# Kernel optimization log

Hardware: AMD Instinct MI355X
Metric: run time of the kernel (lower is better)

## Reference

```python
import jax, jax.numpy as jnp
import numpy as np

B, S, D, H, R, N, RK = 2, 2048, 1024, 16, 64, 32, 128
DH = D // H
EPS = 1e-5


def setup_inputs() -> dict:
    key = jax.random.key(0)
    ks = jax.random.split(key, 24)
    f = lambda i, shape, sc=1.0: jax.random.normal(ks[i], shape, dtype=jnp.float32) * sc
    sm = lambda i, shape: jax.nn.softmax(f(i, shape), axis=-1)
    return {
        'x': f(0, (B, S, D)),
        'f_qk': f(1, (N, D, R), 0.02), 'f_v': f(2, (N, D, R), 0.02),
        'r_qk': f(3, (N, R, D), 0.02), 'r_v': f(4, (N, R, D), 0.02),
        'f_know': f(5, (N, D, RK), 0.02), 'r_know': f(6, (N, RK, D), 0.02),
        'W_O': f(7, (D, D), 0.02),
        'gamma1': jnp.ones(D, jnp.float32), 'beta1': jnp.zeros(D, jnp.float32),
        'gamma2': jnp.ones(D, jnp.float32), 'beta2': jnp.zeros(D, jnp.float32),
        'w_fq': sm(8, (B, S, N)), 'w_fk': sm(9, (B, S, N)), 'w_fv': sm(10, (B, S, N)),
        'w_rq': sm(11, (B, S, N)), 'w_rk': sm(12, (B, S, N)), 'w_rv': sm(13, (B, S, N)),
        'w_know_f': sm(14, (B, S, N)), 'w_know_r': sm(15, (B, S, N)),
    }


def _ln(x, g, b):
    mu = jnp.mean(x, axis=-1, keepdims=True)
    var = jnp.mean(jnp.square(x - mu), axis=-1, keepdims=True)
    return g * (x - mu) * jax.lax.rsqrt(var + EPS) + b


def _feature(x, neurons, w):
    # x [B,S,D], neurons [N,D,R], w [B,S,N] -> [B,S,R]
    all_h = jnp.einsum('bsd,ndr->bsnr', x, neurons)
    return jnp.einsum('bsnr,bsn->bsr', all_h, w)


def _restore(h, neurons, w):
    # h [B,S,R], neurons [N,R,D], w [B,S,N] -> [B,S,D]
    # fuse: avoid materializing [B,S,N,D]; outer-product [B,S,N,R] is small
    t = w[..., None] * h[:, :, None, :]
    return jnp.einsum('bsnr,nrd->bsd', t, neurons)


def _causal_attn(Q, K, V):
    # Q,K,V: [B,H,S,DH]
    scale = 1.0 / jnp.sqrt(jnp.asarray(DH, Q.dtype))
    scores = jnp.einsum('bhqd,bhkd->bhqk', Q, K) * scale
    mask = jnp.tril(jnp.ones((S, S), bool))
    scores = jnp.where(mask, scores, jnp.asarray(-jnp.inf, scores.dtype))
    probs = jax.nn.softmax(scores, axis=-1)
    return jnp.einsum('bhqk,bhkd->bhqd', probs, V)


def reference(x, f_qk, f_v, r_qk, r_v, f_know, r_know, W_O,
              gamma1, beta1, gamma2, beta2,
              w_fq, w_fk, w_fv, w_rq, w_rk, w_rv, w_know_f, w_know_r):
    # --- attention circuit ---
    nx = _ln(x, gamma1, beta1)
    h_q = _feature(nx, f_qk, w_fq)
    h_k = _feature(nx, f_qk, w_fk)
    h_v = _feature(nx, f_v, w_fv)
    Q = _restore(h_q, r_qk, w_rq)
    K = _restore(h_k, r_qk, w_rk)
    V = _restore(h_v, r_v, w_rv)
    to_heads = lambda t: t.reshape(B, S, H, DH).transpose(0, 2, 1, 3)
    attn = _causal_attn(to_heads(Q), to_heads(K), to_heads(V))
    attn = attn.transpose(0, 2, 1, 3).reshape(B, S, D)
    attn_out = attn @ W_O.T  # nn.Linear(d_model, d_model, bias=False)
    x = x + attn_out
    # --- knowledge circuit ---
    nx2 = _ln(x, gamma2, beta2)
    h = _feature(nx2, f_know, w_know_f)
    know_out = _restore(h, r_know, w_know_r)
    x = x + know_out
    return x
```

## Files before the change

kernel.cpp:

```cpp
#include <hip/hip_runtime.h>
#include <stdint.h>


typedef __bf16 bf16x8 __attribute__((ext_vector_type(8)));
typedef float f32x4 __attribute__((ext_vector_type(4)));

__device__ __forceinline__ unsigned short f2b(float f) {
  union { float f; unsigned u; } v; v.f = f;
  unsigned u = v.u;
  unsigned r = (u + 0x7FFFu + ((u >> 16) & 1u)) >> 16;
  return (unsigned short)r;
}
__device__ __forceinline__ float b2f(unsigned short h) {
  union { unsigned u; float f; } v; v.u = ((unsigned)h) << 16;
  return v.f;
}
__device__ __forceinline__ unsigned pk2(float lo, float hi) {
  return (unsigned)f2b(lo) | ((unsigned)f2b(hi) << 16);
}

__global__ __launch_bounds__(256) void gemm_bt(
    const unsigned short* __restrict__ A, const unsigned short* __restrict__ Bt,
    const float* __restrict__ res, void* __restrict__ out,
    int M, int N, int K, int mode, int band) {
  __shared__ unsigned short lsA[128 * 64];
  __shared__ unsigned short lsB[128 * 64];
  const int tid = threadIdx.x;
  const int w = tid >> 6, lane = tid & 63;
  const int quad = lane >> 4, l16 = lane & 15;
  const int wr = w >> 1, wc = w & 1;
  int bx = blockIdx.x, by = blockIdx.y;
  if (band > 0) {
    const int bid = by * gridDim.x + bx;
    const int xcd = bid & 7, j = bid >> 3;
    by = xcd * band + j / gridDim.x;
    bx = j % gridDim.x;
  }
  const int row0 = by * 128;
  const int col0 = bx * 128;

  const int srow = w * 32 + (lane >> 3);
  const int scg = ((lane & 7) ^ (lane >> 3)) * 8;
  const unsigned short* ap = A + (size_t)(row0 + srow) * K + scg;
  const unsigned short* bp = Bt + (size_t)(col0 + srow) * K + scg;

  const f32x4 fz = {0.f, 0.f, 0.f, 0.f};
  f32x4 acc[4][4];
#pragma unroll
  for (int i = 0; i < 4; ++i)
#pragma unroll
    for (int j = 0; j < 4; ++j) acc[i][j] = fz;

  for (int k0 = 0; k0 < K; k0 += 64) {
#pragma unroll
    for (int i = 0; i < 4; ++i) {
      __builtin_amdgcn_global_load_lds(
          (const __attribute__((address_space(1))) unsigned int*)(ap + (size_t)i * 8 * K + k0),
          (__attribute__((address_space(3))) unsigned int*)&lsA[(w * 32 + i * 8) * 64],
          16, 0, 0);
      __builtin_amdgcn_global_load_lds(
          (const __attribute__((address_space(1))) unsigned int*)(bp + (size_t)i * 8 * K + k0),
          (__attribute__((address_space(3))) unsigned int*)&lsB[(w * 32 + i * 8) * 64],
          16, 0, 0);
    }
    __syncthreads();
#pragma unroll
    for (int kk = 0; kk < 2; ++kk) {
      bf16x8 af[4], bfr[4];
      const int sl = (((kk * 4 + quad) ^ (l16 & 7)) * 8);
#pragma unroll
      for (int mt = 0; mt < 4; ++mt)
        af[mt] = *(const bf16x8*)&lsA[(wr * 64 + mt * 16 + l16) * 64 + sl];
#pragma unroll
      for (int nt = 0; nt < 4; ++nt)
        bfr[nt] = *(const bf16x8*)&lsB[(wc * 64 + nt * 16 + l16) * 64 + sl];
#pragma unroll
      for (int mt = 0; mt < 4; ++mt)
#pragma unroll
        for (int nt = 0; nt < 4; ++nt)
          acc[mt][nt] = __builtin_amdgcn_mfma_f32_16x16x32_bf16(af[mt], bfr[nt], acc[mt][nt], 0, 0, 0);
    }
    __syncthreads();
  }

  const int rb = row0 + wr * 64;
  const int cb = col0 + wc * 64;
#pragma unroll
  for (int mt = 0; mt < 4; ++mt) {
#pragma unroll
    for (int nt = 0; nt < 4; ++nt) {
      const int r = rb + mt * 16 + quad * 4;
      const int c = cb + nt * 16 + l16;
#pragma unroll
      for (int i = 0; i < 4; ++i) {
        const float v = acc[mt][nt][i];
        const size_t idx = (size_t)(r + i) * N + c;
        if (mode == 0) ((float*)out)[idx] = v;
        else if (mode == 1) ((unsigned short*)out)[idx] = f2b(v);
        else if (mode == 2) ((float*)out)[idx] = v + res[idx];
        else ((unsigned short*)out)[(size_t)c * M + (r + i)] = f2b(v);
      }
    }
  }
}

__global__ __launch_bounds__(256) void gemm_ks2(
    const unsigned short* __restrict__ A, const unsigned short* __restrict__ Bt,
    float* __restrict__ p0, float* __restrict__ p1, int M, int N, int K) {
  __shared__ unsigned short lsA[128 * 64];
  __shared__ unsigned short lsB[128 * 64];
  const int tid = threadIdx.x;
  const int w = tid >> 6, lane = tid & 63;
  const int quad = lane >> 4, l16 = lane & 15;
  const int wr = w >> 1, wc = w & 1;
  const int nrow8 = (M / 128) >> 3;
  const int bid = blockIdx.y * gridDim.x + blockIdx.x;
  const int xcd = bid & 7, j = bid >> 3;
  const int by = xcd * nrow8 + j / (2 * gridDim.x);
  const int rem = j % (2 * gridDim.x);
  const int ks = rem / gridDim.x;
  const int bx = rem % gridDim.x;
  const int row0 = by * 128;
  const int col0 = bx * 128;
  const int kbeg = ks * (K >> 1), kend = kbeg + (K >> 1);

  const int srow = w * 32 + (lane >> 3);
  const int scg = ((lane & 7) ^ (lane >> 3)) * 8;
  const unsigned short* ap = A + (size_t)(row0 + srow) * K + scg;
  const unsigned short* bp = Bt + (size_t)(col0 + srow) * K + scg;

  const f32x4 fz = {0.f, 0.f, 0.f, 0.f};
  f32x4 acc[4][4];
#pragma unroll
  for (int i = 0; i < 4; ++i)
#pragma unroll
    for (int jj = 0; jj < 4; ++jj) acc[i][jj] = fz;

  for (int k0 = kbeg; k0 < kend; k0 += 64) {
#pragma unroll
    for (int i = 0; i < 4; ++i) {
      __builtin_amdgcn_global_load_lds(
          (const __attribute__((address_space(1))) unsigned int*)(ap + (size_t)i * 8 * K + k0),
          (__attribute__((address_space(3))) unsigned int*)&lsA[(w * 32 + i * 8) * 64],
          16, 0, 0);
      __builtin_amdgcn_global_load_lds(
          (const __attribute__((address_space(1))) unsigned int*)(bp + (size_t)i * 8 * K + k0),
          (__attribute__((address_space(3))) unsigned int*)&lsB[(w * 32 + i * 8) * 64],
          16, 0, 0);
    }
    __syncthreads();
#pragma unroll
    for (int kk = 0; kk < 2; ++kk) {
      bf16x8 af[4], bfr[4];
      const int sl = (((kk * 4 + quad) ^ (l16 & 7)) * 8);
#pragma unroll
      for (int mt = 0; mt < 4; ++mt)
        af[mt] = *(const bf16x8*)&lsA[(wr * 64 + mt * 16 + l16) * 64 + sl];
#pragma unroll
      for (int nt = 0; nt < 4; ++nt)
        bfr[nt] = *(const bf16x8*)&lsB[(wc * 64 + nt * 16 + l16) * 64 + sl];
#pragma unroll
      for (int mt = 0; mt < 4; ++mt)
#pragma unroll
        for (int nt = 0; nt < 4; ++nt)
          acc[mt][nt] = __builtin_amdgcn_mfma_f32_16x16x32_bf16(af[mt], bfr[nt], acc[mt][nt], 0, 0, 0);
    }
    __syncthreads();
  }

  float* out = ks ? p1 : p0;
  const int rb = row0 + wr * 64;
  const int cb = col0 + wc * 64;
#pragma unroll
  for (int mt = 0; mt < 4; ++mt) {
#pragma unroll
    for (int nt = 0; nt < 4; ++nt) {
      const int r = rb + mt * 16 + quad * 4;
      const int c = cb + nt * 16 + l16;
#pragma unroll
      for (int i = 0; i < 4; ++i)
        out[(size_t)(r + i) * N + c] = acc[mt][nt][i];
    }
  }
}

__global__ __launch_bounds__(256) void reduce_add3(
    const float* __restrict__ p0, const float* __restrict__ p1,
    const float* __restrict__ res, float* __restrict__ out, int n) {
  const int i = (blockIdx.x * 256 + threadIdx.x) * 4;
  if (i < n) {
    const f32x4 a = *(const f32x4*)&p0[i];
    const f32x4 b = *(const f32x4*)&p1[i];
    const f32x4 c = *(const f32x4*)&res[i];
    f32x4 o;
#pragma unroll
    for (int k = 0; k < 4; ++k) o[k] = a[k] + b[k] + c[k];
    *(f32x4*)&out[i] = o;
  }
}

__global__ __launch_bounds__(256) void gemm_qkv(
    const unsigned short* __restrict__ t_qk, const unsigned short* __restrict__ t_v,
    const unsigned short* __restrict__ r_qkT, const unsigned short* __restrict__ r_vT,
    unsigned short* __restrict__ QKbuf, unsigned short* __restrict__ VT) {
  __shared__ unsigned short lsA[128 * 64];
  __shared__ unsigned short lsB[128 * 64];
  const int K = 2048;
  const int bid = blockIdx.y * 8 + blockIdx.x;
  const int xcd = bid & 7, j = bid >> 3;
  const int r128 = xcd * 12 + (j >> 3);
  const bool isV = r128 >= 64;
  const unsigned short* A  = isV ? t_v : t_qk;
  const unsigned short* Bt = isV ? r_vT : r_qkT;
  const int row0 = (isV ? r128 - 64 : r128) * 128;
  const int col0 = (j & 7) * 128;
  const int tid = threadIdx.x;
  const int w = tid >> 6, lane = tid & 63;
  const int quad = lane >> 4, l16 = lane & 15;
  const int wr = w >> 1, wc = w & 1;

  const int srow = w * 32 + (lane >> 3);
  const int scg = ((lane & 7) ^ (lane >> 3)) * 8;
  const unsigned short* ap = A + (size_t)(row0 + srow) * K + scg;
  const unsigned short* bp = Bt + (size_t)(col0 + srow) * K + scg;

  const f32x4 fz = {0.f, 0.f, 0.f, 0.f};
  f32x4 acc[4][4];
#pragma unroll
  for (int i = 0; i < 4; ++i)
#pragma unroll
    for (int jj = 0; jj < 4; ++jj) acc[i][jj] = fz;

  for (int k0 = 0; k0 < K; k0 += 64) {
#pragma unroll
    for (int i = 0; i < 4; ++i) {
      __builtin_amdgcn_global_load_lds(
          (const __attribute__((address_space(1))) unsigned int*)(ap + (size_t)i * 8 * K + k0),
          (__attribute__((address_space(3))) unsigned int*)&lsA[(w * 32 + i * 8) * 64],
          16, 0, 0);
      __builtin_amdgcn_global_load_lds(
          (const __attribute__((address_space(1))) unsigned int*)(bp + (size_t)i * 8 * K + k0),
          (__attribute__((address_space(3))) unsigned int*)&lsB[(w * 32 + i * 8) * 64],
          16, 0, 0);
    }
    __syncthreads();
#pragma unroll
    for (int kk = 0; kk < 2; ++kk) {
      bf16x8 af[4], bfr[4];
      const int sl = (((kk * 4 + quad) ^ (l16 & 7)) * 8);
#pragma unroll
      for (int mt = 0; mt < 4; ++mt)
        af[mt] = *(const bf16x8*)&lsA[(wr * 64 + mt * 16 + l16) * 64 + sl];
#pragma unroll
      for (int nt = 0; nt < 4; ++nt)
        bfr[nt] = *(const bf16x8*)&lsB[(wc * 64 + nt * 16 + l16) * 64 + sl];
#pragma unroll
      for (int mt = 0; mt < 4; ++mt)
#pragma unroll
        for (int nt = 0; nt < 4; ++nt)
          acc[mt][nt] = __builtin_amdgcn_mfma_f32_16x16x32_bf16(af[mt], bfr[nt], acc[mt][nt], 0, 0, 0);
    }
    __syncthreads();
  }

  const int rb = row0 + wr * 64;
  const int cb = col0 + wc * 64;
#pragma unroll
  for (int mt = 0; mt < 4; ++mt) {
#pragma unroll
    for (int nt = 0; nt < 4; ++nt) {
      const int r = rb + mt * 16 + quad * 4;
      const int c = cb + nt * 16 + l16;
#pragma unroll
      for (int i = 0; i < 4; ++i) {
        const float v = acc[mt][nt][i];
        if (!isV) QKbuf[(size_t)(r + i) * 1024 + c] = f2b(v);
        else VT[(size_t)c * 4096 + (r + i)] = f2b(v);
      }
    }
  }
}

__global__ __launch_bounds__(256) void ln_kernel(
    const float* __restrict__ x, const float* __restrict__ g,
    const float* __restrict__ be, unsigned short* __restrict__ out) {
  __shared__ float sbuf[4];
  const int t = blockIdx.x, tid = threadIdx.x;
  const float* row = x + (size_t)t * 1024;
  float v[4], s = 0.f;
#pragma unroll
  for (int j = 0; j < 4; ++j) { v[j] = row[tid + j * 256]; s += v[j]; }
#pragma unroll
  for (int off = 32; off; off >>= 1) s += __shfl_xor(s, off);
  if ((tid & 63) == 0) sbuf[tid >> 6] = s;
  __syncthreads();
  const float mu = (sbuf[0] + sbuf[1] + sbuf[2] + sbuf[3]) * (1.f / 1024.f);
  __syncthreads();
  float ss = 0.f;
#pragma unroll
  for (int j = 0; j < 4; ++j) { const float d = v[j] - mu; ss += d * d; }
#pragma unroll
  for (int off = 32; off; off >>= 1) ss += __shfl_xor(ss, off);
  if ((tid & 63) == 0) sbuf[tid >> 6] = ss;
  __syncthreads();
  const float var = (sbuf[0] + sbuf[1] + sbuf[2] + sbuf[3]) * (1.f / 1024.f);
  const float rstd = rsqrtf(var + 1e-5f);
  unsigned short* orow = out + (size_t)t * 1024;
#pragma unroll
  for (int j = 0; j < 4; ++j) {
    const int c = tid + j * 256;
    orow[c] = f2b((v[j] - mu) * rstd * g[c] + be[c]);
  }
}

__global__ __launch_bounds__(256) void mix_attn(
    const unsigned short* __restrict__ all_h,
    const float* __restrict__ w_fq, const float* __restrict__ w_fk,
    const float* __restrict__ w_fv, const float* __restrict__ w_rq,
    const float* __restrict__ w_rk, const float* __restrict__ w_rv,
    unsigned short* __restrict__ t_qk, unsigned short* __restrict__ t_v) {
  __shared__ float hq[64], hk[64], hv[64];
  const int t = blockIdx.x, tid = threadIdx.x;
  const int wv = tid >> 6, lane = tid & 63;
  const unsigned short* row = all_h + (size_t)t * 4096;
  if (wv < 3) {
    const float* wf = (wv == 0 ? w_fq : wv == 1 ? w_fk : w_fv) + (size_t)t * 32;
    const int base = (wv == 2) ? 2048 : 0;
    float acc = 0.f;
#pragma unroll
    for (int n = 0; n < 32; ++n) acc += wf[n] * b2f(row[base + n * 64 + lane]);
    (wv == 0 ? hq : wv == 1 ? hk : hv)[lane] = acc;
  }
  __syncthreads();
  const float* wrq = w_rq + (size_t)t * 32;
  const float* wrk = w_rk + (size_t)t * 32;
  const float* wrv = w_rv + (size_t)t * 32;
  for (int idx = tid; idx < 2048; idx += 256) {
    const int n = idx >> 6, r = idx & 63;
    t_qk[(size_t)t * 2048 + idx] = f2b(wrq[n] * hq[r]);
    t_qk[(size_t)(4096 + t) * 2048 + idx] = f2b(wrk[n] * hk[r]);
    t_v[(size_t)t * 2048 + idx] = f2b(wrv[n] * hv[r]);
  }
}

__global__ __launch_bounds__(256) void mix_know(
    const unsigned short* __restrict__ all_h, const float* __restrict__ w_f,
    const float* __restrict__ w_r, unsigned short* __restrict__ t_know) {
  __shared__ float h[128];
  const int t = blockIdx.x, tid = threadIdx.x;
  const unsigned short* row = all_h + (size_t)t * 4096;
  if (tid < 128) {
    const float* wf = w_f + (size_t)t * 32;
    float acc = 0.f;
#pragma unroll
    for (int n = 0; n < 32; ++n) acc += wf[n] * b2f(row[n * 128 + tid]);
    h[tid] = acc;
  }
  __syncthreads();
  const float* wr = w_r + (size_t)t * 32;
  for (int idx = tid; idx < 4096; idx += 256) {
    const int n = idx >> 7, r = idx & 127;
    t_know[(size_t)t * 4096 + idx] = f2b(wr[n] * h[r]);
  }
}

__global__ __launch_bounds__(256) void transpose_bf(
    const float* __restrict__ in, unsigned short* __restrict__ out, int R, int C) {
  __shared__ float tile[32][33];
  const int bb = blockIdx.z;
  const int c0 = blockIdx.x * 32, r0 = blockIdx.y * 32;
  const int tx = threadIdx.x, ty = threadIdx.y;
  const float* ip = in + (size_t)bb * R * C;
  unsigned short* op = out + (size_t)bb * R * C;
#pragma unroll
  for (int j = 0; j < 4; ++j)
    tile[ty + j * 8][tx] = ip[(size_t)(r0 + ty + j * 8) * C + c0 + tx];
  __syncthreads();
#pragma unroll
  for (int j = 0; j < 4; ++j)
    op[(size_t)(c0 + ty + j * 8) * R + r0 + tx] = f2b(tile[tx][ty + j * 8]);
}

__global__ __launch_bounds__(256) void convert_bf(
    const float* __restrict__ in, unsigned short* __restrict__ out, int n) {
  const int i = blockIdx.x * 256 + threadIdx.x;
  if (i < n) out[i] = f2b(in[i]);
}

__global__ __launch_bounds__(256) void flash_split(
    const unsigned short* __restrict__ Q, const unsigned short* __restrict__ Kp,
    const unsigned short* __restrict__ VT, unsigned short* __restrict__ O,
    float* __restrict__ Opart, float* __restrict__ ml) {
  __shared__ unsigned short Kls[2][64 * 64];
  __shared__ unsigned short Vls[2][64 * 64];
  const int uidx = 79 - (int)blockIdx.x;
  int uu = uidx, qt = 0, ch = 0;
  for (int q = 0; q < 32; ++q) {
    const int n = (q >> 3) + 1;
    if (uu < n) { qt = q; ch = uu; break; }
    uu -= n;
  }
  const int bh = blockIdx.y;
  const int b = bh >> 4, h = bh & 15;
  const int tid = threadIdx.x;
  const int w = tid >> 6, lane = tid & 63, quad = lane >> 4, l16 = lane & 15;
  const int tb = b * 2048;
  const int qrow = qt * 64 + w * 16;
  const int ktlo = ch * 8;
  const int kthi = min(qt, ch * 8 + 7);
  const float C = 0.18033688f;

  const int srow = (lane >> 3);
  const int scol = ((lane & 7) ^ srow) * 8;

  bf16x8 qf[2];
#pragma unroll
  for (int kk = 0; kk < 2; ++kk)
    qf[kk] = *(const bf16x8*)&Q[(size_t)(tb + qrow + l16) * 1024 + h * 64 + kk * 32 + quad * 8];

  const f32x4 fz = {0.f, 0.f, 0.f, 0.f};
  float m_i = -1e30f, l_i = 0.f;
  f32x4 o_acc[4];
#pragma unroll
  for (int nt = 0; nt < 4; ++nt) o_acc[nt] = fz;

  auto stage = [&](int buf, int kt) {
#pragma unroll
    for (int j = 0; j < 2; ++j) {
      const int rg = (w * 2 + j) * 8 + srow;
      __builtin_amdgcn_global_load_lds(
          (const __attribute__((address_space(1))) unsigned int*)
              (Kp + (size_t)(tb + kt * 64 + rg) * 1024 + h * 64 + scol),
          (__attribute__((address_space(3))) unsigned int*)&Kls[buf][(w * 2 + j) * 8 * 64],
          16, 0, 0);
      __builtin_amdgcn_global_load_lds(
          (const __attribute__((address_space(1))) unsigned int*)
              (VT + (size_t)(h * 64 + rg) * 4096 + tb + kt * 64 + scol),
          (__attribute__((address_space(3))) unsigned int*)&Vls[buf][(w * 2 + j) * 8 * 64],
          16, 0, 0);
    }
  };

  const int srcA = (((quad & 1) * 32 + l16) << 2);
  const int srcB = srcA + 64;
  const bool hiq = (quad >= 2);

  stage(0, ktlo);
  __syncthreads();
  int buf = 0;
  for (int kt = ktlo; kt <= kthi; ++kt) {
    bf16x8 kf[8], vf[8];
#pragma unroll
    for (int kk = 0; kk < 2; ++kk)
#pragma unroll
      for (int nt = 0; nt < 4; ++nt) {
        const int sl = (((kk * 4 + quad) ^ (l16 & 7)) * 8);
        kf[kk * 4 + nt] = *(const bf16x8*)&Kls[buf][(nt * 16 + l16) * 64 + sl];
        vf[kk * 4 + nt] = *(const bf16x8*)&Vls[buf][(nt * 16 + l16) * 64 + sl];
      }
    if (kt < kthi) stage(buf ^ 1, kt + 1);

    const bool diag = (kt == qt);
    f32x4 s[4];
#pragma unroll
    for (int nt = 0; nt < 4; ++nt) s[nt] = fz;
#pragma unroll
    for (int kk = 0; kk < 2; ++kk)
#pragma unroll
      for (int nt = 0; nt < 4; ++nt)
        if (!diag || nt <= w)
          s[nt] = __builtin_amdgcn_mfma_f32_16x16x32_bf16(kf[kk * 4 + nt], qf[kk], s[nt], 0, 0, 0);

    const int qloc = w * 16 + l16;
    float mx = -1e30f;
#pragma unroll
    for (int nt = 0; nt < 4; ++nt)
#pragma unroll
      for (int i = 0; i < 4; ++i) {
        float v = s[nt][i];
        if (diag && (nt * 16 + quad * 4 + i) > qloc) v = -1e30f;
        s[nt][i] = v;
        mx = fmaxf(mx, v);
      }
    mx = fmaxf(mx, __shfl_xor(mx, 16));
    mx = fmaxf(mx, __shfl_xor(mx, 32));
    const float mn = fmaxf(m_i, mx);
    const float al = exp2f((m_i - mn) * C);
    m_i = mn;
    const float mC = mn * C;
    float rs = 0.f;
#pragma unroll
    for (int nt = 0; nt < 4; ++nt)
#pragma unroll
      for (int i = 0; i < 4; ++i) {
        const float p = exp2f(fmaf(s[nt][i], C, -mC));
        s[nt][i] = p;
        rs += p;
      }
    rs += __shfl_xor(rs, 16);
    rs += __shfl_xor(rs, 32);
    l_i = l_i * al + rs;
#pragma unroll
    for (int nt = 0; nt < 4; ++nt)
#pragma unroll
      for (int i = 0; i < 4; ++i) o_acc[nt][i] *= al;

    unsigned pk[4][2];
#pragma unroll
    for (int nt = 0; nt < 4; ++nt) {
      pk[nt][0] = pk2(s[nt][0], s[nt][1]);
      pk[nt][1] = pk2(s[nt][2], s[nt][3]);
    }
#pragma unroll
    for (int kk = 0; kk < 2; ++kk) {
      const int ea = 2 * kk, eb = 2 * kk + 1;
      const unsigned u0 = __builtin_amdgcn_ds_bpermute(srcA, pk[ea][0]);
      const unsigned u1 = __builtin_amdgcn_ds_bpermute(srcA, pk[ea][1]);
      const unsigned u2 = __builtin_amdgcn_ds_bpermute(srcB, pk[ea][0]);
      const unsigned u3 = __builtin_amdgcn_ds_bpermute(srcB, pk[ea][1]);
      const unsigned w0 = __builtin_amdgcn_ds_bpermute(srcA, pk[eb][0]);
      const unsigned w1 = __builtin_amdgcn_ds_bpermute(srcA, pk[eb][1]);
      const unsigned w2 = __builtin_amdgcn_ds_bpermute(srcB, pk[eb][0]);
      const unsigned w3 = __builtin_amdgcn_ds_bpermute(srcB, pk[eb][1]);
      unsigned dw[4];
      dw[0] = hiq ? w0 : u0;
      dw[1] = hiq ? w1 : u1;
      dw[2] = hiq ? w2 : u2;
      dw[3] = hiq ? w3 : u3;
      const bf16x8 pf = *(const bf16x8*)dw;
#pragma unroll
      for (int nt = 0; nt < 4; ++nt)
        o_acc[nt] = __builtin_amdgcn_mfma_f32_16x16x32_bf16(vf[kk * 4 + nt], pf, o_acc[nt], 0, 0, 0);
    }
    __syncthreads();
    buf ^= 1;
  }

  const int nch = (qt >> 3) + 1;
  if (nch == 1) {
    const float inv = 1.0f / l_i;
    unsigned short* orow = O + (size_t)(tb + qrow + l16) * 1024 + h * 64;
#pragma unroll
    for (int nt = 0; nt < 4; ++nt) {
      const unsigned d0 = pk2(o_acc[nt][0] * inv, o_acc[nt][1] * inv);
      const unsigned d1 = pk2(o_acc[nt][2] * inv, o_acc[nt][3] * inv);
      *(unsigned*)&orow[nt * 16 + quad * 4] = d0;
      *(unsigned*)&orow[nt * 16 + quad * 4 + 2] = d1;
    }
  } else {
    const int slot = bh * 80 + uidx;
    const int lq = w * 16 + l16;
    float* op = Opart + ((size_t)slot * 64 + lq) * 64;
#pragma unroll
    for (int nt = 0; nt < 4; ++nt)
      *(f32x4*)&op[nt * 16 + quad * 4] = o_acc[nt];
    if (quad == 0) {
      ml[(size_t)slot * 128 + lq * 2] = m_i;
      ml[(size_t)slot * 128 + lq * 2 + 1] = l_i;
    }
  }
}

__global__ __launch_bounds__(256) void flash_reduce(
    const float* __restrict__ Opart, const float* __restrict__ ml,
    unsigned short* __restrict__ O) {
  const int qt = 8 + blockIdx.x;
  const int bh = blockIdx.y;
  const int b = bh >> 4, h = bh & 15;
  const int j = qt >> 3;
  const int base = 8 * (j * (j + 1) / 2) + (qt - 8 * j) * (j + 1);
  const int nch = j + 1;
  const int tid = threadIdx.x;
  const int lq = tid >> 2, dq = (tid & 3) * 16;
  const float C = 0.18033688f;

  float mc[4], lc[4];
  float m = -1e30f;
#pragma unroll
  for (int c = 0; c < 4; ++c) {
    if (c < nch) {
      const size_t sl = (size_t)(bh * 80 + base + c) * 128 + lq * 2;
      mc[c] = ml[sl];
      lc[c] = ml[sl + 1];
    } else { mc[c] = -1e30f; lc[c] = 0.f; }
    m = fmaxf(m, mc[c]);
  }
  float fac[4], lt = 0.f;
#pragma unroll
  for (int c = 0; c < 4; ++c) {
    fac[c] = (c < nch) ? exp2f((mc[c] - m) * C) : 0.f;
    lt += fac[c] * lc[c];
  }
  const float inv = 1.0f / lt;
  float acc[16];
#pragma unroll
  for (int i = 0; i < 16; ++i) acc[i] = 0.f;
#pragma unroll
  for (int c = 0; c < 4; ++c) {
    if (c >= nch) continue;
    const float* op = Opart + ((size_t)(bh * 80 + base + c) * 64 + lq) * 64 + dq;
#pragma unroll
    for (int i = 0; i < 16; i += 4) {
      const f32x4 v = *(const f32x4*)&op[i];
#pragma unroll
      for (int k = 0; k < 4; ++k) acc[i + k] += fac[c] * v[k];
    }
  }
  unsigned short* orow = O + (size_t)(b * 2048 + qt * 64 + lq) * 1024 + h * 64 + dq;
#pragma unroll
  for (int i = 0; i < 16; i += 2)
    *(unsigned*)&orow[i] = pk2(acc[i] * inv, acc[i + 1] * inv);
}

extern "C" void kernel_launch(void* const* d_in, const int* in_sizes, int n_in,
                              void* d_out, int out_size, void* d_ws, size_t ws_size,
                              hipStream_t stream) {
  (void)in_sizes; (void)n_in; (void)out_size; (void)ws_size;
  const float* x      = (const float*)d_in[0];
  const float* f_qk   = (const float*)d_in[1];
  const float* f_v    = (const float*)d_in[2];
  const float* r_qk   = (const float*)d_in[3];
  const float* r_v    = (const float*)d_in[4];
  const float* f_know = (const float*)d_in[5];
  const float* r_know = (const float*)d_in[6];
  const float* W_O    = (const float*)d_in[7];
  const float* gamma1 = (const float*)d_in[8];
  const float* beta1  = (const float*)d_in[9];
  const float* gamma2 = (const float*)d_in[10];
  const float* beta2  = (const float*)d_in[11];
  const float* w_fq   = (const float*)d_in[12];
  const float* w_fk   = (const float*)d_in[13];
  const float* w_fv   = (const float*)d_in[14];
  const float* w_rq   = (const float*)d_in[15];
  const float* w_rk   = (const float*)d_in[16];
  const float* w_rv   = (const float*)d_in[17];
  const float* w_kf   = (const float*)d_in[18];
  const float* w_kr   = (const float*)d_in[19];

  char* base = (char*)d_ws;
  size_t off = 0;
  auto alloc = [&](size_t b) { char* p = base + off; off += (b + 255) & ~(size_t)255; return p; };
  unsigned short* fcomb   = (unsigned short*)alloc(8388608);
  unsigned short* fknowT  = (unsigned short*)alloc(8388608);
  unsigned short* r_qkT   = (unsigned short*)alloc(4194304);
  unsigned short* r_vT    = (unsigned short*)alloc(4194304);
  unsigned short* r_knowT = (unsigned short*)alloc(8388608);
  unsigned short* WO_bf   = (unsigned short*)alloc(2097152);
  unsigned short* nx_bf   = (unsigned short*)alloc(8388608);
  unsigned short* all_h   = (unsigned short*)alloc(33554432);
  unsigned short* t_qk    = (unsigned short*)alloc(33554432);
  unsigned short* t_v     = (unsigned short*)alloc(16777216);
  unsigned short* QKbuf   = (unsigned short*)alloc(16777216);
  unsigned short* VT      = (unsigned short*)alloc(8388608);
  unsigned short* attn    = (unsigned short*)alloc(8388608);
  float* x1 = (float*)t_v;
  float* Opart = (float*)all_h;
  float* mlbuf = (float*)(all_h + 20971520);
  float* pA = (float*)all_h;
  float* pB = (float*)(all_h + 8388608);

  const dim3 blk256(256), blkT(32, 8);

  transpose_bf<<<dim3(2, 32, 32), blkT, 0, stream>>>(f_qk, fcomb, 1024, 64);
  transpose_bf<<<dim3(2, 32, 32), blkT, 0, stream>>>(f_v, fcomb + (size_t)2048 * 1024, 1024, 64);
  transpose_bf<<<dim3(4, 32, 32), blkT, 0, stream>>>(f_know, fknowT, 1024, 128);
  transpose_bf<<<dim3(32, 64, 1), blkT, 0, stream>>>(r_qk, r_qkT, 2048, 1024);
  transpose_bf<<<dim3(32, 64, 1), blkT, 0, stream>>>(r_v, r_vT, 2048, 1024);
  transpose_bf<<<dim3(32, 128, 1), blkT, 0, stream>>>(r_know, r_knowT, 4096, 1024);
  convert_bf<<<4096, blk256, 0, stream>>>(W_O, WO_bf, 1048576);

  ln_kernel<<<4096, blk256, 0, stream>>>(x, gamma1, beta1, nx_bf);
  gemm_bt<<<dim3(32, 32), blk256, 0, stream>>>(nx_bf, fcomb, nullptr, all_h, 4096, 4096, 1024, 1, 0);
  mix_attn<<<4096, blk256, 0, stream>>>(all_h, w_fq, w_fk, w_fv, w_rq, w_rk, w_rv, t_qk, t_v);
  gemm_qkv<<<dim3(8, 96), blk256, 0, stream>>>(t_qk, t_v, r_qkT, r_vT, QKbuf, VT);
  flash_split<<<dim3(80, 32), blk256, 0, stream>>>(QKbuf, QKbuf + (size_t)4096 * 1024, VT, attn,
                                                   Opart, mlbuf);
  flash_reduce<<<dim3(24, 32), blk256, 0, stream>>>(Opart, mlbuf, attn);
  gemm_ks2<<<dim3(8, 64), blk256, 0, stream>>>(attn, WO_bf, pA, pB, 4096, 1024, 1024);
  reduce_add3<<<4096, blk256, 0, stream>>>(pA, pB, x, x1, 4194304);

  ln_kernel<<<4096, blk256, 0, stream>>>(x1, gamma2, beta2, nx_bf);
  gemm_bt<<<dim3(32, 32), blk256, 0, stream>>>(nx_bf, fknowT, nullptr, all_h, 4096, 4096, 1024, 1, 0);
  mix_know<<<4096, blk256, 0, stream>>>(all_h, w_kf, w_kr, t_qk);
  gemm_ks2<<<dim3(8, 64), blk256, 0, stream>>>(t_qk, r_knowT, pA, pB, 4096, 1024, 4096);
  reduce_add3<<<4096, blk256, 0, stream>>>(pA, pB, x1, (float*)d_out, 4194304);
}
```

Before: 570.2 us.

## Split-K the QK, W_O and knowledge GEMMs more and fuse prep kernels

The QK projection GEMM is split into two K halves with bf16 partials plus a reduce kernel, while the V projection stays a full-K GEMM in the same launch. The W_O and knowledge GEMMs go from 2-way to 4-way split-K with fp32 partials and a 5-input reduce-add. The seven weight transpose/convert launches are merged into one prep kernel. The goal is more blocks to fill the CUs and fewer launches. The cost is extra partial-buffer traffic, extra reduce work, and an added bf16 rounding step on the QK partials.

```diff
diff --git a/kernel.cpp b/kernel.cpp
--- a/kernel.cpp
+++ b/kernel.cpp
@@ -21,23 +21,15 @@
 
 __global__ __launch_bounds__(256) void gemm_bt(
     const unsigned short* __restrict__ A, const unsigned short* __restrict__ Bt,
-    const float* __restrict__ res, void* __restrict__ out,
-    int M, int N, int K, int mode, int band) {
+    void* __restrict__ out, int M, int N, int K) {
   __shared__ unsigned short lsA[128 * 64];
   __shared__ unsigned short lsB[128 * 64];
   const int tid = threadIdx.x;
   const int w = tid >> 6, lane = tid & 63;
   const int quad = lane >> 4, l16 = lane & 15;
   const int wr = w >> 1, wc = w & 1;
-  int bx = blockIdx.x, by = blockIdx.y;
-  if (band > 0) {
-    const int bid = by * gridDim.x + bx;
-    const int xcd = bid & 7, j = bid >> 3;
-    by = xcd * band + j / gridDim.x;
-    bx = j % gridDim.x;
-  }
-  const int row0 = by * 128;
-  const int col0 = bx * 128;
+  const int row0 = blockIdx.y * 128;
+  const int col0 = blockIdx.x * 128;
 
   const int srow = w * 32 + (lane >> 3);
   const int scg = ((lane & 7) ^ (lane >> 3)) * 8;
@@ -92,37 +84,42 @@
       const int r = rb + mt * 16 + quad * 4;
       const int c = cb + nt * 16 + l16;
 #pragma unroll
-      for (int i = 0; i < 4; ++i) {
-        const float v = acc[mt][nt][i];
-        const size_t idx = (size_t)(r + i) * N + c;
-        if (mode == 0) ((float*)out)[idx] = v;
-        else if (mode == 1) ((unsigned short*)out)[idx] = f2b(v);
-        else if (mode == 2) ((float*)out)[idx] = v + res[idx];
-        else ((unsigned short*)out)[(size_t)c * M + (r + i)] = f2b(v);
-      }
-    }
-  }
-}
-
-__global__ __launch_bounds__(256) void gemm_ks2(
-    const unsigned short* __restrict__ A, const unsigned short* __restrict__ Bt,
-    float* __restrict__ p0, float* __restrict__ p1, int M, int N, int K) {
+      for (int i = 0; i < 4; ++i)
+        ((unsigned short*)out)[(size_t)(r + i) * N + c] = f2b(acc[mt][nt][i]);
+    }
+  }
+}
+
+__global__ __launch_bounds__(256) void gemm_qkv2(
+    const unsigned short* __restrict__ t_qk, const unsigned short* __restrict__ t_v,
+    const unsigned short* __restrict__ r_qkT, const unsigned short* __restrict__ r_vT,
+    unsigned short* __restrict__ pQK0, unsigned short* __restrict__ pQK1,
+    unsigned short* __restrict__ VT) {
   __shared__ unsigned short lsA[128 * 64];
   __shared__ unsigned short lsB[128 * 64];
+  const int K = 2048;
+  const int bid = blockIdx.x;
+  const unsigned short* A;
+  const unsigned short* Bt;
+  int row0, col0, kbeg, kend, kind;
+  if (bid < 256) {
+    const int xcd = bid & 7, j = bid >> 3;
+    row0 = (xcd * 4 + (j >> 3)) * 128;
+    col0 = (j & 7) * 128;
+    A = t_v; Bt = r_vT; kbeg = 0; kend = K; kind = 0;
+  } else {
+    const int u = bid - 256;
+    const int xcd = u & 7, j = u >> 3;
+    const int row_l = j >> 4, rem = j & 15;
+    const int ks = rem >> 3, col = rem & 7;
+    row0 = (xcd * 8 + row_l) * 128;
+    col0 = col * 128;
+    A = t_qk; Bt = r_qkT; kbeg = ks * 1024; kend = kbeg + 1024; kind = 1 + ks;
+  }
   const int tid = threadIdx.x;
   const int w = tid >> 6, lane = tid & 63;
   const int quad = lane >> 4, l16 = lane & 15;
   const int wr = w >> 1, wc = w & 1;
-  const int nrow8 = (M / 128) >> 3;
-  const int bid = blockIdx.y * gridDim.x + blockIdx.x;
-  const int xcd = bid & 7, j = bid >> 3;
-  const int by = xcd * nrow8 + j / (2 * gridDim.x);
-  const int rem = j % (2 * gridDim.x);
-  const int ks = rem / gridDim.x;
-  const int bx = rem % gridDim.x;
-  const int row0 = by * 128;
-  const int col0 = bx * 128;
-  const int kbeg = ks * (K >> 1), kend = kbeg + (K >> 1);
 
   const int srow = w * 32 + (lane >> 3);
   const int scg = ((lane & 7) ^ (lane >> 3)) * 8;
@@ -168,9 +165,9 @@
     __syncthreads();
   }
 
-  float* out = ks ? p1 : p0;
   const int rb = row0 + wr * 64;
   const int cb = col0 + wc * 64;
+  unsigned short* pout = (kind == 1) ? pQK0 : pQK1;
 #pragma unroll
   for (int mt = 0; mt < 4; ++mt) {
 #pragma unroll
@@ -178,42 +175,48 @@
       const int r = rb + mt * 16 + quad * 4;
       const int c = cb + nt * 16 + l16;
 #pragma unroll
-      for (int i = 0; i < 4; ++i)
-        out[(size_t)(r + i) * N + c] = acc[mt][nt][i];
-    }
-  }
-}
-
-__global__ __launch_bounds__(256) void reduce_add3(
-    const float* __restrict__ p0, const float* __restrict__ p1,
-    const float* __restrict__ res, float* __restrict__ out, int n) {
-  const int i = (blockIdx.x * 256 + threadIdx.x) * 4;
-  if (i < n) {
-    const f32x4 a = *(const f32x4*)&p0[i];
-    const f32x4 b = *(const f32x4*)&p1[i];
-    const f32x4 c = *(const f32x4*)&res[i];
-    f32x4 o;
-#pragma unroll
-    for (int k = 0; k < 4; ++k) o[k] = a[k] + b[k] + c[k];
-    *(f32x4*)&out[i] = o;
-  }
-}
-
-__global__ __launch_bounds__(256) void gemm_qkv(
-    const unsigned short* __restrict__ t_qk, const unsigned short* __restrict__ t_v,
-    const unsigned short* __restrict__ r_qkT, const unsigned short* __restrict__ r_vT,
-    unsigned short* __restrict__ QKbuf, unsigned short* __restrict__ VT) {
+      for (int i = 0; i < 4; ++i) {
+        const float v = acc[mt][nt][i];
+        if (kind == 0) VT[(size_t)c * 4096 + (r + i)] = f2b(v);
+        else pout[(size_t)(r + i) * 1024 + c] = f2b(v);
+      }
+    }
+  }
+}
+
+__global__ __launch_bounds__(256) void reduce_qk(
+    const unsigned short* __restrict__ p0, const unsigned short* __restrict__ p1,
+    unsigned short* __restrict__ out) {
+  const int i = (blockIdx.x * 256 + threadIdx.x) * 8;
+  uint4 a = *(const uint4*)&p0[i];
+  uint4 b = *(const uint4*)&p1[i];
+  unsigned r[4];
+  const unsigned* aa = (const unsigned*)&a;
+  const unsigned* bb = (const unsigned*)&b;
+#pragma unroll
+  for (int k = 0; k < 4; ++k) {
+    const float lo = b2f((unsigned short)(aa[k] & 0xFFFF)) + b2f((unsigned short)(bb[k] & 0xFFFF));
+    const float hi = b2f((unsigned short)(aa[k] >> 16)) + b2f((unsigned short)(bb[k] >> 16));
+    r[k] = pk2(lo, hi);
+  }
+  *(uint4*)&out[i] = *(uint4*)r;
+}
+
+__global__ __launch_bounds__(256) void gemm_ks4(
+    const unsigned short* __restrict__ A, const unsigned short* __restrict__ Bt,
+    float* __restrict__ p0, float* __restrict__ p1,
+    float* __restrict__ p2, float* __restrict__ p3, int K) {
   __shared__ unsigned short lsA[128 * 64];
   __shared__ unsigned short lsB[128 * 64];
-  const int K = 2048;
-  const int bid = blockIdx.y * 8 + blockIdx.x;
+  const int N = 1024;
+  const int bid = blockIdx.x;
   const int xcd = bid & 7, j = bid >> 3;
-  const int r128 = xcd * 12 + (j >> 3);
-  const bool isV = r128 >= 64;
-  const unsigned short* A  = isV ? t_v : t_qk;
-  const unsigned short* Bt = isV ? r_vT : r_qkT;
-  const int row0 = (isV ? r128 - 64 : r128) * 128;
-  const int col0 = (j & 7) * 128;
+  const int row_l = j >> 5, rem = j & 31;
+  const int ks = rem >> 3, col = rem & 7;
+  const int row0 = (xcd * 4 + row_l) * 128;
+  const int col0 = col * 128;
+  const int kq = K >> 2;
+  const int kbeg = ks * kq, kend = kbeg + kq;
   const int tid = threadIdx.x;
   const int w = tid >> 6, lane = tid & 63;
   const int quad = lane >> 4, l16 = lane & 15;
@@ -231,7 +234,7 @@
 #pragma unroll
     for (int jj = 0; jj < 4; ++jj) acc[i][jj] = fz;
 
-  for (int k0 = 0; k0 < K; k0 += 64) {
+  for (int k0 = kbeg; k0 < kend; k0 += 64) {
 #pragma unroll
     for (int i = 0; i < 4; ++i) {
       __builtin_amdgcn_global_load_lds(
@@ -263,6 +266,7 @@
     __syncthreads();
   }
 
+  float* out = (ks == 0) ? p0 : (ks == 1) ? p1 : (ks == 2) ? p2 : p3;
   const int rb = row0 + wr * 64;
   const int cb = col0 + wc * 64;
 #pragma unroll
@@ -272,13 +276,26 @@
       const int r = rb + mt * 16 + quad * 4;
       const int c = cb + nt * 16 + l16;
 #pragma unroll
-      for (int i = 0; i < 4; ++i) {
-        const float v = acc[mt][nt][i];
-        if (!isV) QKbuf[(size_t)(r + i) * 1024 + c] = f2b(v);
-        else VT[(size_t)c * 4096 + (r + i)] = f2b(v);
-      }
-    }
-  }
+      for (int i = 0; i < 4; ++i)
+        out[(size_t)(r + i) * N + c] = acc[mt][nt][i];
+    }
+  }
+}
+
+__global__ __launch_bounds__(256) void reduce_add5(
+    const float* __restrict__ p0, const float* __restrict__ p1,
+    const float* __restrict__ p2, const float* __restrict__ p3,
+    const float* __restrict__ res, float* __restrict__ out) {
+  const int i = (blockIdx.x * 256 + threadIdx.x) * 4;
+  const f32x4 a = *(const f32x4*)&p0[i];
+  const f32x4 b = *(const f32x4*)&p1[i];
+  const f32x4 c = *(const f32x4*)&p2[i];
+  const f32x4 d = *(const f32x4*)&p3[i];
+  const f32x4 e = *(const f32x4*)&res[i];
+  f32x4 o;
+#pragma unroll
+  for (int k = 0; k < 4; ++k) o[k] = ((a[k] + b[k]) + (c[k] + d[k])) + e[k];
+  *(f32x4*)&out[i] = o;
 }
 
 __global__ __launch_bounds__(256) void ln_kernel(
@@ -364,12 +381,36 @@
   }
 }
 
-__global__ __launch_bounds__(256) void transpose_bf(
-    const float* __restrict__ in, unsigned short* __restrict__ out, int R, int C) {
+__global__ __launch_bounds__(256) void prep_all(
+    const float* __restrict__ f_qk, const float* __restrict__ f_v,
+    const float* __restrict__ f_know, const float* __restrict__ r_qk,
+    const float* __restrict__ r_v, const float* __restrict__ r_know,
+    const float* __restrict__ W_O,
+    unsigned short* __restrict__ fcomb, unsigned short* __restrict__ fknowT,
+    unsigned short* __restrict__ r_qkT, unsigned short* __restrict__ r_vT,
+    unsigned short* __restrict__ r_knowT, unsigned short* __restrict__ WO_bf) {
   __shared__ float tile[32][33];
-  const int bb = blockIdx.z;
-  const int c0 = blockIdx.x * 32, r0 = blockIdx.y * 32;
+  const int bid = blockIdx.x;
   const int tx = threadIdx.x, ty = threadIdx.y;
+  const float* in;
+  unsigned short* out;
+  int R, C, gx, loc;
+  if (bid < 2048)       { in = f_qk;   out = fcomb;                         R = 1024; C = 64;   gx = 2;  loc = bid; }
+  else if (bid < 4096)  { in = f_v;    out = fcomb + (size_t)2048 * 1024;   R = 1024; C = 64;   gx = 2;  loc = bid - 2048; }
+  else if (bid < 8192)  { in = f_know; out = fknowT;                        R = 1024; C = 128;  gx = 4;  loc = bid - 4096; }
+  else if (bid < 10240) { in = r_qk;   out = r_qkT;                         R = 2048; C = 1024; gx = 32; loc = bid - 8192; }
+  else if (bid < 12288) { in = r_v;    out = r_vT;                          R = 2048; C = 1024; gx = 32; loc = bid - 10240; }
+  else if (bid < 16384) { in = r_know; out = r_knowT;                       R = 4096; C = 1024; gx = 32; loc = bid - 12288; }
+  else {
+    const int i = ((bid - 16384) * 256 + ty * 32 + tx) * 4;
+    const f32x4 v = *(const f32x4*)&W_O[i];
+    *(unsigned*)&WO_bf[i] = pk2(v[0], v[1]);
+    *(unsigned*)&WO_bf[i + 2] = pk2(v[2], v[3]);
+    return;
+  }
+  const int tiles = gx * (R >> 5);
+  const int bb = loc / tiles, rem = loc % tiles;
+  const int r0 = (rem / gx) * 32, c0 = (rem % gx) * 32;
   const float* ip = in + (size_t)bb * R * C;
   unsigned short* op = out + (size_t)bb * R * C;
 #pragma unroll
@@ -379,12 +420,6 @@
 #pragma unroll
   for (int j = 0; j < 4; ++j)
     op[(size_t)(c0 + ty + j * 8) * R + r0 + tx] = f2b(tile[tx][ty + j * 8]);
-}
-
-__global__ __launch_bounds__(256) void convert_bf(
-    const float* __restrict__ in, unsigned short* __restrict__ out, int n) {
-  const int i = blockIdx.x * 256 + threadIdx.x;
-  if (i < n) out[i] = f2b(in[i]);
 }
 
 __global__ __launch_bounds__(256) void flash_split(
@@ -654,34 +689,36 @@
   unsigned short* VT      = (unsigned short*)alloc(8388608);
   unsigned short* attn    = (unsigned short*)alloc(8388608);
   float* x1 = (float*)t_v;
+  unsigned short* pQK0 = all_h;
+  unsigned short* pQK1 = all_h + 8388608;
   float* Opart = (float*)all_h;
-  float* mlbuf = (float*)(all_h + 20971520);
-  float* pA = (float*)all_h;
-  float* pB = (float*)(all_h + 8388608);
+  float* mlbuf = (float*)((char*)all_h + 41943040);
+  float* pW0 = (float*)all_h;
+  float* pW1 = (float*)((char*)all_h + 16777216);
+  float* pW2 = (float*)QKbuf;
+  float* pW3 = (float*)VT;
+  float* pW3_wo   = (float*)t_qk;
+  float* pW3_know = (float*)VT;
 
   const dim3 blk256(256), blkT(32, 8);
 
-  transpose_bf<<<dim3(2, 32, 32), blkT, 0, stream>>>(f_qk, fcomb, 1024, 64);
-  transpose_bf<<<dim3(2, 32, 32), blkT, 0, stream>>>(f_v, fcomb + (size_t)2048 * 1024, 1024, 64);
-  transpose_bf<<<dim3(4, 32, 32), blkT, 0, stream>>>(f_know, fknowT, 1024, 128);
-  transpose_bf<<<dim3(32, 64, 1), blkT, 0, stream>>>(r_qk, r_qkT, 2048, 1024);
-  transpose_bf<<<dim3(32, 64, 1), blkT, 0, stream>>>(r_v, r_vT, 2048, 1024);
-  transpose_bf<<<dim3(32, 128, 1), blkT, 0, stream>>>(r_know, r_knowT, 4096, 1024);
-  convert_bf<<<4096, blk256, 0, stream>>>(W_O, WO_bf, 1048576);
+  prep_all<<<17408, blkT, 0, stream>>>(f_qk, f_v, f_know, r_qk, r_v, r_know, W_O,
+                                       fcomb, fknowT, r_qkT, r_vT, r_knowT, WO_bf);
 
   ln_kernel<<<4096, blk256, 0, stream>>>(x, gamma1, beta1, nx_bf);
-  gemm_bt<<<dim3(32, 32), blk256, 0, stream>>>(nx_bf, fcomb, nullptr, all_h, 4096, 4096, 1024, 1, 0);
+  gemm_bt<<<dim3(32, 32), blk256, 0, stream>>>(nx_bf, fcomb, all_h, 4096, 4096, 1024);
   mix_attn<<<4096, blk256, 0, stream>>>(all_h, w_fq, w_fk, w_fv, w_rq, w_rk, w_rv, t_qk, t_v);
-  gemm_qkv<<<dim3(8, 96), blk256, 0, stream>>>(t_qk, t_v, r_qkT, r_vT, QKbuf, VT);
+  gemm_qkv2<<<1280, blk256, 0, stream>>>(t_qk, t_v, r_qkT, r_vT, pQK0, pQK1, VT);
+  reduce_qk<<<4096, blk256, 0, stream>>>(pQK0, pQK1, QKbuf);
   flash_split<<<dim3(80, 32), blk256, 0, stream>>>(QKbuf, QKbuf + (size_t)4096 * 1024, VT, attn,
                                                    Opart, mlbuf);
   flash_reduce<<<dim3(24, 32), blk256, 0, stream>>>(Opart, mlbuf, attn);
-  gemm_ks2<<<dim3(8, 64), blk256, 0, stream>>>(attn, WO_bf, pA, pB, 4096, 1024, 1024);
-  reduce_add3<<<4096, blk256, 0, stream>>>(pA, pB, x, x1, 4194304);
+  gemm_ks4<<<1024, blk256, 0, stream>>>(attn, WO_bf, pW0, pW1, pW2, pW3_wo, 1024);
+  reduce_add5<<<4096, blk256, 0, stream>>>(pW0, pW1, pW2, pW3_wo, x, x1);
 
   ln_kernel<<<4096, blk256, 0, stream>>>(x1, gamma2, beta2, nx_bf);
-  gemm_bt<<<dim3(32, 32), blk256, 0, stream>>>(nx_bf, fknowT, nullptr, all_h, 4096, 4096, 1024, 1, 0);
+  gemm_bt<<<dim3(32, 32), blk256, 0, stream>>>(nx_bf, fknowT, all_h, 4096, 4096, 1024);
   mix_know<<<4096, blk256, 0, stream>>>(all_h, w_kf, w_kr, t_qk);
-  gemm_ks2<<<dim3(8, 64), blk256, 0, stream>>>(t_qk, r_knowT, pA, pB, 4096, 1024, 4096);
-  reduce_add3<<<4096, blk256, 0, stream>>>(pA, pB, x1, (float*)d_out, 4194304);
-}
+  gemm_ks4<<<1024, blk256, 0, stream>>>(t_qk, r_knowT, pW0, pW1, pW2, pW3_know, 4096);
+  reduce_add5<<<4096, blk256, 0, stream>>>(pW0, pW1, pW2, pW3_know, x1, (float*)d_out);
+}
```

Result: faster. 552.6 us (-3.1%).
